# Optimization experiments

Measured on AMD Instinct MI355X. Metric: run time of the kernel, lower is better.

The kernel has to match this reference:

```python
import jax, jax.numpy as jnp
import numpy as np

B, S, E = 8, 1024, 512      # batch, seq, emb_size
L, H, K, F = 2, 4, 4, 128    # blocks, heads, conv kernel, final_size
I = 2 * E                    # inner dim (proj_factor=2)
DH = I // H                  # head dim
EPS = 1e-5


def _layernorm(x, g, b):
    mu = jnp.mean(x, axis=-1, keepdims=True)
    var = jnp.var(x, axis=-1, keepdims=True)
    return (x - mu) * jax.lax.rsqrt(var + EPS) * g + b


def _causal_conv(x, w, b):
    # x: [B,S,I], w: [K,I] depthwise, left-padded causal conv
    y = jax.lax.conv_general_dilated(
        x, w[:, None, :], window_strides=(1,), padding=[(K - 1, 0)],
        dimension_numbers=('NWC', 'WIO', 'NWC'), feature_group_count=I)
    return y + b


def _mlstm_parallel(q, k, v, ipre, fpre):
    # q,k,v: [B,H,S,DH]; ipre,fpre: [B,H,S]  (stabilized parallel mLSTM)
    lf = jax.nn.log_sigmoid(fpre)                       # [B,H,S]
    lfc = jnp.cumsum(lf, axis=-1)
    logD = lfc[..., :, None] - lfc[..., None, :] + ipre[..., None, :]  # [B,H,S,S]
    mask = jnp.tril(jnp.ones((S, S), dtype=bool))
    logD = jnp.where(mask, logD, -jnp.inf)
    m = jnp.max(logD, axis=-1, keepdims=True)           # [B,H,S,1]
    Dm = jnp.exp(logD - m)
    scores = jnp.einsum('bhtd,bhsd->bhts', q, k) * (DH ** -0.5) * Dm
    n = jnp.maximum(jnp.abs(jnp.sum(scores, axis=-1, keepdims=True)), jnp.exp(-m))
    return jnp.einsum('bhts,bhsd->bhtd', scores, v) / n


def _block(x, ln_g, ln_b, w_up, conv_w, conv_b, wq, wk, wv,
           w_i, b_i, w_f, b_f, skip, gn_g, w_down, b_down):
    res = x
    xn = _layernorm(x, ln_g, ln_b)
    up = xn @ w_up                                      # [B,S,2I]
    x_m, z = up[..., :I], up[..., I:]
    c_act = jax.nn.silu(_causal_conv(x_m, conv_w, conv_b))
    q = c_act @ wq
    k = c_act @ wk
    v = x_m @ wv
    qkv = jnp.concatenate([q, k, v], axis=-1)           # [B,S,3I]
    ipre = jnp.transpose(qkv @ w_i + b_i, (0, 2, 1))    # [B,H,S]
    fpre = jnp.transpose(qkv @ w_f + b_f, (0, 2, 1))
    to_h = lambda t: jnp.transpose(t.reshape(B, S, H, DH), (0, 2, 1, 3))
    h = _mlstm_parallel(to_h(q), to_h(k), to_h(v), ipre, fpre)  # [B,H,S,DH]
    # per-head group norm
    mu = jnp.mean(h, axis=-1, keepdims=True)
    var = jnp.var(h, axis=-1, keepdims=True)
    h = (h - mu) * jax.lax.rsqrt(var + EPS)
    h = jnp.transpose(h, (0, 2, 1, 3)).reshape(B, S, I) * gn_g
    h = h + skip * c_act
    h = h * jax.nn.silu(z)
    return res + h @ w_down + b_down


def setup_inputs() -> dict:
    key = jax.random.key(0)
    ks = jax.random.split(key, 12)
    n = lambda k, shp, s=0.02: jax.random.normal(k, shp, jnp.float32) * s
    return {
        'x': jax.random.normal(ks[0], (B, S, E), jnp.float32),
        'ln_g': jnp.ones((L, E), jnp.float32), 'ln_b': jnp.zeros((L, E), jnp.float32),
        'w_up': n(ks[1], (L, E, 2 * I)),
        'conv_w': n(ks[2], (L, K, I), 0.1), 'conv_b': jnp.zeros((L, I), jnp.float32),
        'wq': n(ks[3], (L, I, I)), 'wk': n(ks[4], (L, I, I)), 'wv': n(ks[5], (L, I, I)),
        'w_i': n(ks[6], (L, 3 * I, H)), 'b_i': jnp.zeros((L, H), jnp.float32),
        'w_f': n(ks[7], (L, 3 * I, H)), 'b_f': 3.0 * jnp.ones((L, H), jnp.float32),
        'skip': jnp.ones((L, I), jnp.float32), 'gn_g': jnp.ones((L, I), jnp.float32),
        'w_down': n(ks[8], (L, I, E)), 'b_down': jnp.zeros((L, E), jnp.float32),
        'w_fin': n(ks[9], (E, F)), 'b_fin': jnp.zeros((F,), jnp.float32),
    }


def reference(x, ln_g, ln_b, w_up, conv_w, conv_b, wq, wk, wv, w_i, b_i,
              w_f, b_f, skip, gn_g, w_down, b_down, w_fin, b_fin):
    h = x
    for l in range(L):  # 2 structurally identical mLSTM blocks
        h = _block(h, ln_g[l], ln_b[l], w_up[l], conv_w[l], conv_b[l],
                   wq[l], wk[l], wv[l], w_i[l], b_i[l], w_f[l], b_f[l],
                   skip[l], gn_g[l], w_down[l], b_down[l])
    return h @ w_fin + b_fin
```

## Files before the change

kernel.cpp:

```cpp
#include <hip/hip_runtime.h>
#include <math.h>

#define S_LEN 1024
#define I_DIM 1024
#define DH_   256
#define H_NUM 4
#define B_NUM 8
#define ROWS  (B_NUM*S_LEN)

#define GLOBAL_AS __attribute__((address_space(1)))
#define LDS_AS    __attribute__((address_space(3)))

#define VM0    asm volatile("s_waitcnt vmcnt(0)" ::: "memory")
#define LGKM0  asm volatile("s_waitcnt lgkmcnt(0)" ::: "memory")
#define BAR    __builtin_amdgcn_s_barrier()
#define SFENCE __builtin_amdgcn_sched_barrier(0)

typedef __attribute__((ext_vector_type(8))) short bf16x8;
typedef __attribute__((ext_vector_type(4))) float f32x4;
typedef unsigned short u16;

__device__ __forceinline__ u16 f2bf(float f) {
    union { float f; unsigned u; } v; v.f = f;
    unsigned r = v.u + 0x7FFF + ((v.u >> 16) & 1);
    return (u16)(r >> 16);
}
__device__ __forceinline__ float bf2f(u16 h) {
    union { unsigned u; float f; } v; v.u = ((unsigned)h) << 16;
    return v.f;
}

__global__ __launch_bounds__(64) void ln_fused_k(const float* __restrict__ x,
                                                 const float* __restrict__ g,
                                                 const float* __restrict__ b,
                                                 u16* __restrict__ out) {
    int row = blockIdx.x, lane = threadIdx.x;
    const float* xr = x + (size_t)row * 512;
    float4 a = *(const float4*)&xr[lane * 8];
    float4 c = *(const float4*)&xr[lane * 8 + 4];
    float s  = a.x + a.y + a.z + a.w + c.x + c.y + c.z + c.w;
    float s2 = a.x*a.x + a.y*a.y + a.z*a.z + a.w*a.w
             + c.x*c.x + c.y*c.y + c.z*c.z + c.w*c.w;
#pragma unroll
    for (int off = 32; off > 0; off >>= 1) {
        s  += __shfl_down(s, off);
        s2 += __shfl_down(s2, off);
    }
    s = __shfl(s, 0); s2 = __shfl(s2, 0);
    float mu = s * (1.f / 512.f);
    float rstd = rsqrtf(s2 * (1.f / 512.f) - mu * mu + 1e-5f);
    int e0 = lane * 8;
    float y[8] = {a.x,a.y,a.z,a.w,c.x,c.y,c.z,c.w};
    ushort4 o0, o1;
    o0.x = f2bf((y[0]-mu)*rstd*g[e0+0]+b[e0+0]);
    o0.y = f2bf((y[1]-mu)*rstd*g[e0+1]+b[e0+1]);
    o0.z = f2bf((y[2]-mu)*rstd*g[e0+2]+b[e0+2]);
    o0.w = f2bf((y[3]-mu)*rstd*g[e0+3]+b[e0+3]);
    o1.x = f2bf((y[4]-mu)*rstd*g[e0+4]+b[e0+4]);
    o1.y = f2bf((y[5]-mu)*rstd*g[e0+5]+b[e0+5]);
    o1.z = f2bf((y[6]-mu)*rstd*g[e0+6]+b[e0+6]);
    o1.w = f2bf((y[7]-mu)*rstd*g[e0+7]+b[e0+7]);
    *(ushort4*)&out[(size_t)row * 512 + e0]     = o0;
    *(ushort4*)&out[(size_t)row * 512 + e0 + 4] = o1;
}

__global__ __launch_bounds__(256) void cvtT_k(const float* __restrict__ W,
                                              u16* __restrict__ Wt, int K, int N) {
    __shared__ float t[32][33];
    int k0 = blockIdx.x * 32, n0 = blockIdx.y * 32;
    int c = threadIdx.x & 31, r8 = threadIdx.x >> 5;
#pragma unroll
    for (int q = 0; q < 4; q++) {
        int r = r8 * 4 + q;
        t[r][c] = W[(size_t)(k0 + r) * N + n0 + c];
    }
    __syncthreads();
#pragma unroll
    for (int q = 0; q < 4; q++) {
        int r = r8 * 4 + q;
        Wt[(size_t)(n0 + r) * K + k0 + c] = f2bf(t[c][r]);
    }
}

__global__ __launch_bounds__(256) void vt_k(const u16* __restrict__ v,
                                            u16* __restrict__ vt) {
    __shared__ u16 t[32][34];
    int s0 = blockIdx.x * 32, d0 = blockIdx.y * 32, bh = blockIdx.z;
    int b = bh >> 2, h = bh & 3;
    int c = threadIdx.x & 31, r4 = threadIdx.x >> 5;
#pragma unroll
    for (int q = 0; q < 4; q++) {
        int r = r4 * 4 + q;
        t[r][c] = v[(size_t)(b * 1024 + s0 + r) * I_DIM + h * 256 + d0 + c];
    }
    __syncthreads();
#pragma unroll
    for (int q = 0; q < 4; q++) {
        int r = r4 * 4 + q;
        vt[((size_t)bh * 256 + d0 + r) * 1024 + s0 + c] = t[c][r];
    }
}

template<int EPI>
__global__ __launch_bounds__(256) void gemm_bf16_k(
    const u16* __restrict__ A, const u16* __restrict__ Wt, int N, int K,
    float* __restrict__ Cf, u16* __restrict__ Cb,
    const float* __restrict__ bias, const float* __restrict__ res, int ldres)
{
    __shared__ __align__(16) u16 As[2][128 * 32];
    __shared__ __align__(16) u16 Bs[2][128 * 32];
    int tid = threadIdx.x;
    int lane = tid & 63;
    int wm = (tid >> 6) & 1, wn = tid >> 7;
    int gx = gridDim.x;
    int nwg = gx * gridDim.y;
    int bid = blockIdx.y * gx + blockIdx.x;
    int cpx = nwg >> 3;
    int swz = (bid & 7) * cpx + (bid >> 3);
    int r0 = (swz / gx) * 128, n0 = (swz % gx) * 128;

    int arow = tid >> 2, acol = (tid & 3) * 8;
    const u16* ap0 = A  + (size_t)(r0 + arow) * K + acol;
    const u16* ap1 = A  + (size_t)(r0 + 64 + arow) * K + acol;
    const u16* bp0 = Wt + (size_t)(n0 + arow) * K + acol;
    const u16* bp1 = Wt + (size_t)(n0 + 64 + arow) * K + acol;

    auto stage = [&](int kt, int bs) {
        int koff = kt * 32;
        __builtin_amdgcn_global_load_lds((const GLOBAL_AS unsigned int*)(ap0 + koff), (LDS_AS unsigned int*)&As[bs][tid * 8], 16, 0, 0);
        __builtin_amdgcn_global_load_lds((const GLOBAL_AS unsigned int*)(ap1 + koff), (LDS_AS unsigned int*)&As[bs][2048 + tid * 8], 16, 0, 0);
        __builtin_amdgcn_global_load_lds((const GLOBAL_AS unsigned int*)(bp0 + koff), (LDS_AS unsigned int*)&Bs[bs][tid * 8], 16, 0, 0);
        __builtin_amdgcn_global_load_lds((const GLOBAL_AS unsigned int*)(bp1 + koff), (LDS_AS unsigned int*)&Bs[bs][2048 + tid * 8], 16, 0, 0);
    };

    f32x4 acc[4][4];
#pragma unroll
    for (int i = 0; i < 4; i++)
#pragma unroll
        for (int j = 0; j < 4; j++) acc[i][j] = (f32x4){0.f, 0.f, 0.f, 0.f};

    int lm = lane & 15, lk = (lane >> 4) * 8;
    int nt = K >> 5;
    stage(0, 0);
    VM0; BAR; SFENCE;
    for (int t = 0; t < nt; ++t) {
        int cur = t & 1;
        if (t + 1 < nt) stage(t + 1, cur ^ 1);
        bf16x8 af[4], bfr[4];
#pragma unroll
        for (int f = 0; f < 4; f++) {
            af[f]  = *(const bf16x8*)&As[cur][(wm * 64 + f * 16 + lm) * 32 + lk];
            bfr[f] = *(const bf16x8*)&Bs[cur][(wn * 64 + f * 16 + lm) * 32 + lk];
        }
#pragma unroll
        for (int i = 0; i < 4; i++)
#pragma unroll
            for (int j = 0; j < 4; j++)
                acc[i][j] = __builtin_amdgcn_mfma_f32_16x16x32_bf16(af[i], bfr[j], acc[i][j], 0, 0, 0);
        VM0; BAR; SFENCE;
    }
    int lr = (lane >> 4) * 4;
#pragma unroll
    for (int i = 0; i < 4; i++) {
#pragma unroll
        for (int j = 0; j < 4; j++) {
#pragma unroll
            for (int q = 0; q < 4; q++) {
                int row = r0 + wm * 64 + i * 16 + lr + q;
                int col = n0 + wn * 64 + j * 16 + lm;
                float o = acc[i][j][q];
                if (EPI == 0) {
                    Cb[(size_t)row * N + col] = f2bf(o);
                } else if (EPI == 1) {
                    if (col < 1024) Cb[(size_t)row * 1024 + col] = f2bf(o);
                    else            Cf[(size_t)row * 1024 + (col - 1024)] = o;
                } else if (EPI == 2) {
                    o += bias[col] + res[(size_t)row * ldres + col];
                    Cf[(size_t)row * N + col] = o;
                    Cb[(size_t)row * N + col] = f2bf(o);
                } else {
                    o += bias[col];
                    Cf[(size_t)row * N + col] = o;
                }
            }
        }
    }
}

__global__ __launch_bounds__(256) void conv_k(const u16* __restrict__ xm,
                                              const float* __restrict__ w,
                                              const float* __restrict__ cb,
                                              u16* __restrict__ cact) {
    int idx = blockIdx.x * 256 + threadIdx.x;
    int r = idx >> 8;
    int c = (idx & 255) * 4;
    int t = r & 1023;
    const u16* base = xm + (size_t)(r - t) * I_DIM;
    float4 acc = *(const float4*)&cb[c];
#pragma unroll
    for (int j = 0; j < 4; j++) {
        int tt = t - 3 + j;
        if (tt >= 0) {
            short4 s = *(const short4*)&base[(size_t)tt * I_DIM + c];
            float4 wv = *(const float4*)&w[j * I_DIM + c];
            acc.x = fmaf(bf2f((u16)s.x), wv.x, acc.x);
            acc.y = fmaf(bf2f((u16)s.y), wv.y, acc.y);
            acc.z = fmaf(bf2f((u16)s.z), wv.z, acc.z);
            acc.w = fmaf(bf2f((u16)s.w), wv.w, acc.w);
        }
    }
    acc.x = acc.x / (1.f + __expf(-acc.x));
    acc.y = acc.y / (1.f + __expf(-acc.y));
    acc.z = acc.z / (1.f + __expf(-acc.z));
    acc.w = acc.w / (1.f + __expf(-acc.w));
    ushort4 o;
    o.x = f2bf(acc.x); o.y = f2bf(acc.y); o.z = f2bf(acc.z); o.w = f2bf(acc.w);
    *(ushort4*)&cact[(size_t)r * I_DIM + c] = o;
}

__global__ __launch_bounds__(256) void gates_k(const u16* __restrict__ q,
                                               const u16* __restrict__ k,
                                               const u16* __restrict__ v,
                                               const float* __restrict__ wi,
                                               const float* __restrict__ bi,
                                               const float* __restrict__ wf,
                                               const float* __restrict__ bf,
                                               float* __restrict__ ipre,
                                               float* __restrict__ fpre) {
    int r0 = blockIdx.x * 4;
    int tid = threadIdx.x;
    float ai[4][4], af4[4][4];
#pragma unroll
    for (int r = 0; r < 4; r++)
#pragma unroll
        for (int m = 0; m < 4; m++) { ai[r][m] = 0.f; af4[r][m] = 0.f; }
#pragma unroll
    for (int part = 0; part < 3; part++) {
        const u16* src = (part == 0 ? q : (part == 1 ? k : v)) + (size_t)r0 * I_DIM;
        const float* wip = wi + part * I_DIM * 4;
        const float* wfp = wf + part * I_DIM * 4;
#pragma unroll
        for (int jj = 0; jj < 4; jj++) {
            int e = tid + jj * 256;
            float4 w4  = *(const float4*)&wip[e * 4];
            float4 f4v = *(const float4*)&wfp[e * 4];
#pragma unroll
            for (int r = 0; r < 4; r++) {
                float xv = bf2f(src[(size_t)r * I_DIM + e]);
                ai[r][0] = fmaf(xv, w4.x, ai[r][0]);
                ai[r][1] = fmaf(xv, w4.y, ai[r][1]);
                ai[r][2] = fmaf(xv, w4.z, ai[r][2]);
                ai[r][3] = fmaf(xv, w4.w, ai[r][3]);
                af4[r][0] = fmaf(xv, f4v.x, af4[r][0]);
                af4[r][1] = fmaf(xv, f4v.y, af4[r][1]);
                af4[r][2] = fmaf(xv, f4v.z, af4[r][2]);
                af4[r][3] = fmaf(xv, f4v.w, af4[r][3]);
            }
        }
    }
#pragma unroll
    for (int off = 32; off > 0; off >>= 1) {
#pragma unroll
        for (int r = 0; r < 4; r++)
#pragma unroll
            for (int m = 0; m < 4; m++) {
                ai[r][m]  += __shfl_down(ai[r][m], off);
                af4[r][m] += __shfl_down(af4[r][m], off);
            }
    }
    __shared__ float red[4][32];
    int wv_ = tid >> 6, lane = tid & 63;
    if (lane == 0) {
#pragma unroll
        for (int r = 0; r < 4; r++)
#pragma unroll
            for (int m = 0; m < 4; m++) {
                red[wv_][r * 8 + m]     = ai[r][m];
                red[wv_][r * 8 + 4 + m] = af4[r][m];
            }
    }
    __syncthreads();
    if (tid < 32) {
        int r = tid >> 3, m = tid & 7;
        float s_ = red[0][tid] + red[1][tid] + red[2][tid] + red[3][tid];
        int row = r0 + r, bb = row >> 10, ss = row & 1023;
        if (m < 4) ipre[((size_t)(bb * 4 + m)) * 1024 + ss] = s_ + bi[m];
        else       fpre[((size_t)(bb * 4 + (m - 4))) * 1024 + ss] = s_ + bf[m - 4];
    }
}

__global__ __launch_bounds__(1024) void scan_k(const float* __restrict__ ipre,
                                               const float* __restrict__ fpre,
                                               float* __restrict__ cA,
                                               float* __restrict__ MA,
                                               float* __restrict__ nF) {
    __shared__ float buf[1024];
    int bh = blockIdx.x, t = threadIdx.x;
    size_t base = (size_t)bh * 1024;
    float fp = fpre[base + t];
    float lf = (fp >= 0.f) ? -log1pf(expf(-fp)) : (fp - log1pf(expf(fp)));
    buf[t] = lf; __syncthreads();
    for (int off = 1; off < 1024; off <<= 1) {
        float u = (t >= off) ? buf[t - off] : 0.f;
        __syncthreads();
        buf[t] += u;
        __syncthreads();
    }
    float lfc = buf[t];
    float c = ipre[base + t] - lfc;
    __syncthreads();
    buf[t] = c; __syncthreads();
    for (int off = 1; off < 1024; off <<= 1) {
        float u = (t >= off) ? buf[t - off] : -3.4e38f;
        __syncthreads();
        buf[t] = fmaxf(buf[t], u);
        __syncthreads();
    }
    float M = buf[t];
    cA[base + t] = c * 1.44269504f;
    MA[base + t] = M * 1.44269504f;
    nF[base + t] = expf(-(lfc + M));
}

__global__ __launch_bounds__(256) void attn_k(
    const u16* __restrict__ qg, const u16* __restrict__ kg, const u16* __restrict__ vt,
    const float* __restrict__ c2A, const float* __restrict__ M2A, const float* __restrict__ nFl,
    const u16* __restrict__ cact, const float* __restrict__ zb, u16* __restrict__ hb,
    const float* __restrict__ gng, const float* __restrict__ skip)
{
    __shared__ __align__(16) u16 Kb[2][32 * 256];
    __shared__ __align__(16) u16 Ps[64 * 40];
    __shared__ float rsI[64];
    __shared__ float gS[64 * 4];
    __shared__ float gQ[64 * 4];
    __shared__ float gmu[64], gvr[64];

    int tid = threadIdx.x;
    int w = tid >> 6, l = tid & 63;
    int lm = l & 15, lk = l >> 4;
    int b = blockIdx.z, h = blockIdx.y;
    int T0 = (15 - blockIdx.x) * 64;
    int bh32 = b * H_NUM + h;
    size_t bh = (size_t)bh32 * S_LEN;

    bf16x8 qf[8];
    {
        size_t base = ((size_t)(b * S_LEN + T0 + w * 16 + lm)) * I_DIM + h * DH_ + lk * 8;
#pragma unroll
        for (int ks = 0; ks < 8; ks++) qf[ks] = *(const bf16x8*)&qg[base + ks * 32];
    }
    f32x4 acc[4][4];
#pragma unroll
    for (int i = 0; i < 4; i++)
#pragma unroll
        for (int jd = 0; jd < 4; jd++) acc[i][jd] = (f32x4){0.f, 0.f, 0.f, 0.f};
    float rsum[2][4] = {{0,0,0,0},{0,0,0,0}};
    float m2r[4]; int tg[4];
#pragma unroll
    for (int q = 0; q < 4; q++) {
        tg[q] = T0 + w * 16 + lk * 4 + q;
        m2r[q] = M2A[bh + tg[q]];
    }

    const size_t krow0 = ((size_t)(b * S_LEN)) * I_DIM + h * DH_;
    const u16* vptr = vt + (size_t)bh32 * 256 * S_LEN + (size_t)(w * 64 + lm) * S_LEN + lk * 8;

    auto stageK = [&](int s0, int bs) {
#pragma unroll
        for (int r = 0; r < 4; r++) {
            int q = r * 256 + tid;
            int row = q >> 5, cl = q & 31;
            int cs = cl ^ (row & 7);
            const u16* src = kg + krow0 + (size_t)(s0 + row) * I_DIM + cs * 8;
            __builtin_amdgcn_global_load_lds((const GLOBAL_AS unsigned int*)src,
                                             (LDS_AS unsigned int*)&Kb[bs][q * 8], 16, 0, 0);
        }
    };

    int nst = (T0 >> 5) + 2;
    stageK(0, 0);
    bf16x8 vA[4], vB[4];
    float c2c[2], c2n[2];
#pragma unroll
    for (int jd = 0; jd < 4; jd++) vA[jd] = *(const bf16x8*)(vptr + jd * 16 * S_LEN);
    c2c[0] = c2A[bh + lm];
    c2c[1] = c2A[bh + 16 + lm];
    VM0; BAR; SFENCE;

    for (int st = 0; st < nst; st++) {
        int s0 = st * 32;
        int cur = st & 1;
        int more = (st + 1 < nst);
        if (more) {
            stageK(s0 + 32, cur ^ 1);
#pragma unroll
            for (int jd = 0; jd < 4; jd++) vB[jd] = *(const bf16x8*)(vptr + jd * 16 * S_LEN + s0 + 32);
            c2n[0] = c2A[bh + s0 + 32 + lm];
            c2n[1] = c2A[bh + s0 + 48 + lm];
        }
        f32x4 sacc[2];
        sacc[0] = (f32x4){0.f,0.f,0.f,0.f};
        sacc[1] = (f32x4){0.f,0.f,0.f,0.f};
        __builtin_amdgcn_s_setprio(1);
#pragma unroll
        for (int ks = 0; ks < 8; ks++) {
#pragma unroll
            for (int js = 0; js < 2; js++) {
                int row = js * 16 + lm;
                int ch = (ks * 4 + lk) ^ (row & 7);
                bf16x8 kf = *(const bf16x8*)&Kb[cur][row * 256 + ch * 8];
                sacc[js] = __builtin_amdgcn_mfma_f32_16x16x32_bf16(qf[ks], kf, sacc[js], 0, 0, 0);
            }
        }
        __builtin_amdgcn_s_setprio(0);
#pragma unroll
        for (int js = 0; js < 2; js++) {
            int sg = s0 + js * 16 + lm;
#pragma unroll
            for (int q = 0; q < 4; q++) {
                float v = sacc[js][q] * 0.0625f * __builtin_amdgcn_exp2f(c2c[js] - m2r[q]);
                v = (sg <= tg[q]) ? v : 0.f;
                u16 pb = f2bf(v);
                rsum[js][q] += bf2f(pb);
                Ps[(w * 16 + lk * 4 + q) * 40 + js * 16 + lm] = pb;
            }
        }
        LGKM0; BAR; SFENCE;
        __builtin_amdgcn_s_setprio(1);
#pragma unroll
        for (int i = 0; i < 4; i++) {
            bf16x8 pa = *(const bf16x8*)&Ps[(i * 16 + lm) * 40 + lk * 8];
#pragma unroll
            for (int jd = 0; jd < 4; jd++)
                acc[i][jd] = __builtin_amdgcn_mfma_f32_16x16x32_bf16(pa, vA[jd], acc[i][jd], 0, 0, 0);
        }
        __builtin_amdgcn_s_setprio(0);
        VM0; BAR; SFENCE;
        if (more) {
#pragma unroll
            for (int jd = 0; jd < 4; jd++) vA[jd] = vB[jd];
            c2c[0] = c2n[0]; c2c[1] = c2n[1];
        }
    }
    {
        float rq[4];
#pragma unroll
        for (int q = 0; q < 4; q++) rq[q] = rsum[0][q] + rsum[1][q];
#pragma unroll
        for (int m = 1; m < 16; m <<= 1) {
#pragma unroll
            for (int q = 0; q < 4; q++) rq[q] += __shfl_xor(rq[q], m);
        }
        if (lm == 0) {
#pragma unroll
            for (int q = 0; q < 4; q++) rsI[w * 16 + lk * 4 + q] = rq[q];
        }
    }
    __syncthreads();
    if (tid < 64) {
        float n = fmaxf(fabsf(rsI[tid]), nFl[bh + T0 + tid]);
        rsI[tid] = 1.f / n;
    }
    __syncthreads();
#pragma unroll
    for (int i = 0; i < 4; i++) {
#pragma unroll
        for (int q = 0; q < 4; q++) {
            int rl = i * 16 + lk * 4 + q;
            float inv = rsI[rl];
            float ps = 0.f, pq = 0.f;
#pragma unroll
            for (int jd = 0; jd < 4; jd++) {
                float v = acc[i][jd][q] * inv;
                acc[i][jd][q] = v;
                ps += v; pq += v * v;
            }
#pragma unroll
            for (int m = 1; m < 16; m <<= 1) {
                ps += __shfl_xor(ps, m);
                pq += __shfl_xor(pq, m);
            }
            if (lm == 0) { gS[rl * 4 + w] = ps; gQ[rl * 4 + w] = pq; }
        }
    }
    __syncthreads();
    if (tid < 64) {
        float s1 = gS[tid*4] + gS[tid*4+1] + gS[tid*4+2] + gS[tid*4+3];
        float s2 = gQ[tid*4] + gQ[tid*4+1] + gQ[tid*4+2] + gQ[tid*4+3];
        float mu = s1 * (1.f / 256.f);
        float var = s2 * (1.f / 256.f) - mu * mu;
        gmu[tid] = mu;
        gvr[tid] = rsqrtf(var + 1e-5f);
    }
    __syncthreads();
#pragma unroll
    for (int i = 0; i < 4; i++) {
#pragma unroll
        for (int q = 0; q < 4; q++) {
            int rl = i * 16 + lk * 4 + q;
            size_t r = (size_t)b * S_LEN + T0 + rl;
            float mu = gmu[rl], rv = gvr[rl];
#pragma unroll
            for (int jd = 0; jd < 4; jd++) {
                int cix = h * DH_ + w * 64 + jd * 16 + lm;
                float val = (acc[i][jd][q] - mu) * rv * gng[cix];
                float ca = bf2f(cact[r * I_DIM + cix]);
                float z = zb[r * I_DIM + cix];
                float hm = (val + skip[cix] * ca) * (z / (1.f + __expf(-z)));
                hb[r * I_DIM + cix] = f2bf(hm);
            }
        }
    }
}

extern "C" void kernel_launch(void* const* d_in, const int* in_sizes, int n_in,
                              void* d_out, int out_size, void* d_ws, size_t ws_size,
                              hipStream_t stream) {
    const float* x      = (const float*)d_in[0];
    const float* ln_g   = (const float*)d_in[1];
    const float* ln_b   = (const float*)d_in[2];
    const float* w_up   = (const float*)d_in[3];
    const float* conv_w = (const float*)d_in[4];
    const float* conv_b = (const float*)d_in[5];
    const float* wq     = (const float*)d_in[6];
    const float* wk     = (const float*)d_in[7];
    const float* wv     = (const float*)d_in[8];
    const float* w_i    = (const float*)d_in[9];
    const float* b_i    = (const float*)d_in[10];
    const float* w_f    = (const float*)d_in[11];
    const float* b_f    = (const float*)d_in[12];
    const float* skip   = (const float*)d_in[13];
    const float* gn_g   = (const float*)d_in[14];
    const float* w_down = (const float*)d_in[15];
    const float* b_down = (const float*)d_in[16];
    const float* w_fin  = (const float*)d_in[17];
    const float* b_fin  = (const float*)d_in[18];

    char* p = (char*)d_ws;
    auto alloc = [&](size_t bytes) { void* r = p; p += (bytes + 255) & ~(size_t)255; return r; };
    float* zbuf  = (float*)alloc((size_t)ROWS * 1024 * 4);
    float* xa    = (float*)alloc((size_t)ROWS * 512 * 4);
    float* xb2   = (float*)alloc((size_t)ROWS * 512 * 4);
    u16*  xln    = (u16*)alloc((size_t)ROWS * 512 * 2);
    u16*  xm     = (u16*)alloc((size_t)ROWS * 1024 * 2);
    u16*  cactb  = (u16*)alloc((size_t)ROWS * 1024 * 2);
    u16*  qbf    = (u16*)alloc((size_t)ROWS * 1024 * 2);
    u16*  kbf    = (u16*)alloc((size_t)ROWS * 1024 * 2);
    u16*  vbf    = (u16*)alloc((size_t)ROWS * 1024 * 2);
    u16*  vtg    = (u16*)alloc((size_t)32 * 256 * 1024 * 2);
    u16*  hbf    = (u16*)alloc((size_t)ROWS * 1024 * 2);
    u16*  xoutb  = (u16*)alloc((size_t)ROWS * 512 * 2);
    u16*  wupT   = (u16*)alloc((size_t)2 * 2048 * 512 * 2);
    u16*  wqT    = (u16*)alloc((size_t)2 * 1024 * 1024 * 2);
    u16*  wkT    = (u16*)alloc((size_t)2 * 1024 * 1024 * 2);
    u16*  wvT    = (u16*)alloc((size_t)2 * 1024 * 1024 * 2);
    u16*  wdT    = (u16*)alloc((size_t)2 * 512 * 1024 * 2);
    u16*  wfT    = (u16*)alloc((size_t)128 * 512 * 2);
    float* ipre  = (float*)alloc(32768 * 4);
    float* fpre  = (float*)alloc(32768 * 4);
    float* cA    = (float*)alloc(32768 * 4);
    float* MA    = (float*)alloc(32768 * 4);
    float* nF    = (float*)alloc(32768 * 4);

    for (int l = 0; l < 2; l++) {
        cvtT_k<<<dim3(16, 64), 256, 0, stream>>>(w_up + (size_t)l * 512 * 2048, wupT + (size_t)l * 2048 * 512, 512, 2048);
        cvtT_k<<<dim3(32, 32), 256, 0, stream>>>(wq + (size_t)l * 1024 * 1024, wqT + (size_t)l * 1024 * 1024, 1024, 1024);
        cvtT_k<<<dim3(32, 32), 256, 0, stream>>>(wk + (size_t)l * 1024 * 1024, wkT + (size_t)l * 1024 * 1024, 1024, 1024);
        cvtT_k<<<dim3(32, 32), 256, 0, stream>>>(wv + (size_t)l * 1024 * 1024, wvT + (size_t)l * 1024 * 1024, 1024, 1024);
        cvtT_k<<<dim3(32, 16), 256, 0, stream>>>(w_down + (size_t)l * 1024 * 512, wdT + (size_t)l * 512 * 1024, 1024, 512);
    }
    cvtT_k<<<dim3(16, 4), 256, 0, stream>>>(w_fin, wfT, 512, 128);

    const float* xin = x;
    for (int l = 0; l < 2; l++) {
        float* xout = (l == 0) ? xa : xb2;
        ln_fused_k<<<ROWS, 64, 0, stream>>>(xin, ln_g + l * 512, ln_b + l * 512, xln);
        gemm_bf16_k<1><<<dim3(16, 64), 256, 0, stream>>>(
            xln, wupT + (size_t)l * 2048 * 512, 2048, 512, zbuf, xm, nullptr, nullptr, 0);
        conv_k<<<ROWS, 256, 0, stream>>>(xm, conv_w + l * 4 * I_DIM, conv_b + l * I_DIM, cactb);
        gemm_bf16_k<0><<<dim3(8, 64), 256, 0, stream>>>(
            xm, wvT + (size_t)l * 1024 * 1024, 1024, 1024, nullptr, vbf, nullptr, nullptr, 0);
        gemm_bf16_k<0><<<dim3(8, 64), 256, 0, stream>>>(
            cactb, wqT + (size_t)l * 1024 * 1024, 1024, 1024, nullptr, qbf, nullptr, nullptr, 0);
        gemm_bf16_k<0><<<dim3(8, 64), 256, 0, stream>>>(
            cactb, wkT + (size_t)l * 1024 * 1024, 1024, 1024, nullptr, kbf, nullptr, nullptr, 0);
        vt_k<<<dim3(32, 8, 32), 256, 0, stream>>>(vbf, vtg);
        gates_k<<<ROWS / 4, 256, 0, stream>>>(qbf, kbf, vbf,
            w_i + l * 3072 * 4, b_i + l * 4, w_f + l * 3072 * 4, b_f + l * 4, ipre, fpre);
        scan_k<<<32, 1024, 0, stream>>>(ipre, fpre, cA, MA, nF);
        attn_k<<<dim3(16, 4, 8), 256, 0, stream>>>(qbf, kbf, vtg, cA, MA, nF, cactb, zbuf, hbf,
            gn_g + l * I_DIM, skip + l * I_DIM);
        gemm_bf16_k<2><<<dim3(4, 64), 256, 0, stream>>>(
            hbf, wdT + (size_t)l * 512 * 1024, 512, 1024, xout, xoutb,
            b_down + l * 512, xin, 512);
        xin = xout;
    }
    gemm_bf16_k<3><<<dim3(1, 64), 256, 0, stream>>>(
        xoutb, wfT, 128, 512, (float*)d_out, nullptr, b_fin, nullptr, 0);
}
```

Before: 693.9 us.

## Fuse Q/K projections into one GEMM and halve attention query tile

```diff
diff --git a/kernel.cpp b/kernel.cpp
--- a/kernel.cpp
+++ b/kernel.cpp
@@ -218,8 +218,7 @@
     *(ushort4*)&cact[(size_t)r * I_DIM + c] = o;
 }
 
-__global__ __launch_bounds__(256) void gates_k(const u16* __restrict__ q,
-                                               const u16* __restrict__ k,
+__global__ __launch_bounds__(256) void gates_k(const u16* __restrict__ qk,
                                                const u16* __restrict__ v,
                                                const float* __restrict__ wi,
                                                const float* __restrict__ bi,
@@ -236,7 +235,10 @@
         for (int m = 0; m < 4; m++) { ai[r][m] = 0.f; af4[r][m] = 0.f; }
 #pragma unroll
     for (int part = 0; part < 3; part++) {
-        const u16* src = (part == 0 ? q : (part == 1 ? k : v)) + (size_t)r0 * I_DIM;
+        const u16* src; size_t st;
+        if (part == 0)      { src = qk + (size_t)r0 * 2048;        st = 2048; }
+        else if (part == 1) { src = qk + (size_t)r0 * 2048 + 1024; st = 2048; }
+        else                { src = v  + (size_t)r0 * 1024;        st = 1024; }
         const float* wip = wi + part * I_DIM * 4;
         const float* wfp = wf + part * I_DIM * 4;
 #pragma unroll
@@ -246,7 +248,7 @@
             float4 f4v = *(const float4*)&wfp[e * 4];
 #pragma unroll
             for (int r = 0; r < 4; r++) {
-                float xv = bf2f(src[(size_t)r * I_DIM + e]);
+                float xv = bf2f(src[(size_t)r * st + e]);
                 ai[r][0] = fmaf(xv, w4.x, ai[r][0]);
                 ai[r][1] = fmaf(xv, w4.y, ai[r][1]);
                 ai[r][2] = fmaf(xv, w4.z, ai[r][2]);
@@ -329,40 +331,44 @@
     const float* __restrict__ gng, const float* __restrict__ skip)
 {
     __shared__ __align__(16) u16 Kb[2][32 * 256];
-    __shared__ __align__(16) u16 Ps[64 * 40];
-    __shared__ float rsI[64];
-    __shared__ float gS[64 * 4];
-    __shared__ float gQ[64 * 4];
-    __shared__ float gmu[64], gvr[64];
+    __shared__ __align__(16) u16 Ps[32 * 40];
+    __shared__ float rs2[4][16];
+    __shared__ float rsI[32];
+    __shared__ float gS[32 * 4];
+    __shared__ float gQ[32 * 4];
+    __shared__ float gmu[32], gvr[32];
 
     int tid = threadIdx.x;
     int w = tid >> 6, l = tid & 63;
     int lm = l & 15, lk = l >> 4;
-    int b = blockIdx.z, h = blockIdx.y;
-    int T0 = (15 - blockIdx.x) * 64;
+    int i0 = blockIdx.x;
+    int g = (i0 & 7) * 128 + (i0 >> 3);
+    int b = g >> 7, h = (g >> 5) & 3, bx = g & 31;
+    int T0 = (31 - bx) * 32;
+    int tf = w & 1, sf = w >> 1;
     int bh32 = b * H_NUM + h;
     size_t bh = (size_t)bh32 * S_LEN;
 
     bf16x8 qf[8];
     {
-        size_t base = ((size_t)(b * S_LEN + T0 + w * 16 + lm)) * I_DIM + h * DH_ + lk * 8;
+        size_t base = ((size_t)(b * S_LEN + T0 + tf * 16 + lm)) * 2048 + h * DH_ + lk * 8;
 #pragma unroll
         for (int ks = 0; ks < 8; ks++) qf[ks] = *(const bf16x8*)&qg[base + ks * 32];
     }
-    f32x4 acc[4][4];
-#pragma unroll
-    for (int i = 0; i < 4; i++)
+    f32x4 acc[2][4];
+#pragma unroll
+    for (int i = 0; i < 2; i++)
 #pragma unroll
         for (int jd = 0; jd < 4; jd++) acc[i][jd] = (f32x4){0.f, 0.f, 0.f, 0.f};
-    float rsum[2][4] = {{0,0,0,0},{0,0,0,0}};
+    float rsum[4] = {0, 0, 0, 0};
     float m2r[4]; int tg[4];
 #pragma unroll
     for (int q = 0; q < 4; q++) {
-        tg[q] = T0 + w * 16 + lk * 4 + q;
+        tg[q] = T0 + tf * 16 + lk * 4 + q;
         m2r[q] = M2A[bh + tg[q]];
     }
 
-    const size_t krow0 = ((size_t)(b * S_LEN)) * I_DIM + h * DH_;
+    const size_t krow0 = (size_t)(b * S_LEN) * 2048 + h * DH_;
     const u16* vptr = vt + (size_t)bh32 * 256 * S_LEN + (size_t)(w * 64 + lm) * S_LEN + lk * 8;
 
     auto stageK = [&](int s0, int bs) {
@@ -371,20 +377,19 @@
             int q = r * 256 + tid;
             int row = q >> 5, cl = q & 31;
             int cs = cl ^ (row & 7);
-            const u16* src = kg + krow0 + (size_t)(s0 + row) * I_DIM + cs * 8;
+            const u16* src = kg + krow0 + (size_t)(s0 + row) * 2048 + cs * 8;
             __builtin_amdgcn_global_load_lds((const GLOBAL_AS unsigned int*)src,
                                              (LDS_AS unsigned int*)&Kb[bs][q * 8], 16, 0, 0);
         }
     };
 
-    int nst = (T0 >> 5) + 2;
+    int nst = (T0 >> 5) + 1;
     stageK(0, 0);
     bf16x8 vA[4], vB[4];
-    float c2c[2], c2n[2];
+    float c2c, c2n;
 #pragma unroll
     for (int jd = 0; jd < 4; jd++) vA[jd] = *(const bf16x8*)(vptr + jd * 16 * S_LEN);
-    c2c[0] = c2A[bh + lm];
-    c2c[1] = c2A[bh + 16 + lm];
+    c2c = c2A[bh + sf * 16 + lm];
     VM0; BAR; SFENCE;
 
     for (int st = 0; st < nst; st++) {
@@ -395,40 +400,33 @@
             stageK(s0 + 32, cur ^ 1);
 #pragma unroll
             for (int jd = 0; jd < 4; jd++) vB[jd] = *(const bf16x8*)(vptr + jd * 16 * S_LEN + s0 + 32);
-            c2n[0] = c2A[bh + s0 + 32 + lm];
-            c2n[1] = c2A[bh + s0 + 48 + lm];
-        }
-        f32x4 sacc[2];
-        sacc[0] = (f32x4){0.f,0.f,0.f,0.f};
-        sacc[1] = (f32x4){0.f,0.f,0.f,0.f};
+            c2n = c2A[bh + s0 + 32 + sf * 16 + lm];
+        }
+        f32x4 sacc = (f32x4){0.f, 0.f, 0.f, 0.f};
         __builtin_amdgcn_s_setprio(1);
 #pragma unroll
         for (int ks = 0; ks < 8; ks++) {
-#pragma unroll
-            for (int js = 0; js < 2; js++) {
-                int row = js * 16 + lm;
-                int ch = (ks * 4 + lk) ^ (row & 7);
-                bf16x8 kf = *(const bf16x8*)&Kb[cur][row * 256 + ch * 8];
-                sacc[js] = __builtin_amdgcn_mfma_f32_16x16x32_bf16(qf[ks], kf, sacc[js], 0, 0, 0);
-            }
+            int row = sf * 16 + lm;
+            int ch = (ks * 4 + lk) ^ (row & 7);
+            bf16x8 kf = *(const bf16x8*)&Kb[cur][row * 256 + ch * 8];
+            sacc = __builtin_amdgcn_mfma_f32_16x16x32_bf16(qf[ks], kf, sacc, 0, 0, 0);
         }
         __builtin_amdgcn_s_setprio(0);
-#pragma unroll
-        for (int js = 0; js < 2; js++) {
-            int sg = s0 + js * 16 + lm;
+        {
+            int sg = s0 + sf * 16 + lm;
 #pragma unroll
             for (int q = 0; q < 4; q++) {
-                float v = sacc[js][q] * 0.0625f * __builtin_amdgcn_exp2f(c2c[js] - m2r[q]);
+                float v = sacc[q] * 0.0625f * __builtin_amdgcn_exp2f(c2c - m2r[q]);
                 v = (sg <= tg[q]) ? v : 0.f;
                 u16 pb = f2bf(v);
-                rsum[js][q] += bf2f(pb);
-                Ps[(w * 16 + lk * 4 + q) * 40 + js * 16 + lm] = pb;
+                rsum[q] += bf2f(pb);
+                Ps[(tf * 16 + lk * 4 + q) * 40 + sf * 16 + lm] = pb;
             }
         }
         LGKM0; BAR; SFENCE;
         __builtin_amdgcn_s_setprio(1);
 #pragma unroll
-        for (int i = 0; i < 4; i++) {
+        for (int i = 0; i < 2; i++) {
             bf16x8 pa = *(const bf16x8*)&Ps[(i * 16 + lm) * 40 + lk * 8];
 #pragma unroll
             for (int jd = 0; jd < 4; jd++)
@@ -439,31 +437,30 @@
         if (more) {
 #pragma unroll
             for (int jd = 0; jd < 4; jd++) vA[jd] = vB[jd];
-            c2c[0] = c2n[0]; c2c[1] = c2n[1];
+            c2c = c2n;
         }
     }
     {
-        float rq[4];
-#pragma unroll
-        for (int q = 0; q < 4; q++) rq[q] = rsum[0][q] + rsum[1][q];
 #pragma unroll
         for (int m = 1; m < 16; m <<= 1) {
 #pragma unroll
-            for (int q = 0; q < 4; q++) rq[q] += __shfl_xor(rq[q], m);
+            for (int q = 0; q < 4; q++) rsum[q] += __shfl_xor(rsum[q], m);
         }
         if (lm == 0) {
 #pragma unroll
-            for (int q = 0; q < 4; q++) rsI[w * 16 + lk * 4 + q] = rq[q];
-        }
-    }
-    __syncthreads();
-    if (tid < 64) {
-        float n = fmaxf(fabsf(rsI[tid]), nFl[bh + T0 + tid]);
+            for (int q = 0; q < 4; q++) rs2[w][lk * 4 + q] = rsum[q];
+        }
+    }
+    __syncthreads();
+    if (tid < 32) {
+        int tfi = tid >> 4, idx = tid & 15;
+        float s = rs2[tfi][idx] + rs2[tfi + 2][idx];
+        float n = fmaxf(fabsf(s), nFl[bh + T0 + tid]);
         rsI[tid] = 1.f / n;
     }
     __syncthreads();
 #pragma unroll
-    for (int i = 0; i < 4; i++) {
+    for (int i = 0; i < 2; i++) {
 #pragma unroll
         for (int q = 0; q < 4; q++) {
             int rl = i * 16 + lk * 4 + q;
@@ -484,7 +481,7 @@
         }
     }
     __syncthreads();
-    if (tid < 64) {
+    if (tid < 32) {
         float s1 = gS[tid*4] + gS[tid*4+1] + gS[tid*4+2] + gS[tid*4+3];
         float s2 = gQ[tid*4] + gQ[tid*4+1] + gQ[tid*4+2] + gQ[tid*4+3];
         float mu = s1 * (1.f / 256.f);
@@ -494,7 +491,7 @@
     }
     __syncthreads();
 #pragma unroll
-    for (int i = 0; i < 4; i++) {
+    for (int i = 0; i < 2; i++) {
 #pragma unroll
         for (int q = 0; q < 4; q++) {
             int rl = i * 16 + lk * 4 + q;
@@ -544,15 +541,13 @@
     u16*  xln    = (u16*)alloc((size_t)ROWS * 512 * 2);
     u16*  xm     = (u16*)alloc((size_t)ROWS * 1024 * 2);
     u16*  cactb  = (u16*)alloc((size_t)ROWS * 1024 * 2);
-    u16*  qbf    = (u16*)alloc((size_t)ROWS * 1024 * 2);
-    u16*  kbf    = (u16*)alloc((size_t)ROWS * 1024 * 2);
+    u16*  qkbf   = (u16*)alloc((size_t)ROWS * 2048 * 2);
     u16*  vbf    = (u16*)alloc((size_t)ROWS * 1024 * 2);
     u16*  vtg    = (u16*)alloc((size_t)32 * 256 * 1024 * 2);
     u16*  hbf    = (u16*)alloc((size_t)ROWS * 1024 * 2);
     u16*  xoutb  = (u16*)alloc((size_t)ROWS * 512 * 2);
     u16*  wupT   = (u16*)alloc((size_t)2 * 2048 * 512 * 2);
-    u16*  wqT    = (u16*)alloc((size_t)2 * 1024 * 1024 * 2);
-    u16*  wkT    = (u16*)alloc((size_t)2 * 1024 * 1024 * 2);
+    u16*  wqkT   = (u16*)alloc((size_t)2 * 2048 * 1024 * 2);
     u16*  wvT    = (u16*)alloc((size_t)2 * 1024 * 1024 * 2);
     u16*  wdT    = (u16*)alloc((size_t)2 * 512 * 1024 * 2);
     u16*  wfT    = (u16*)alloc((size_t)128 * 512 * 2);
@@ -564,8 +559,8 @@
 
     for (int l = 0; l < 2; l++) {
         cvtT_k<<<dim3(16, 64), 256, 0, stream>>>(w_up + (size_t)l * 512 * 2048, wupT + (size_t)l * 2048 * 512, 512, 2048);
-        cvtT_k<<<dim3(32, 32), 256, 0, stream>>>(wq + (size_t)l * 1024 * 1024, wqT + (size_t)l * 1024 * 1024, 1024, 1024);
-        cvtT_k<<<dim3(32, 32), 256, 0, stream>>>(wk + (size_t)l * 1024 * 1024, wkT + (size_t)l * 1024 * 1024, 1024, 1024);
+        cvtT_k<<<dim3(32, 32), 256, 0, stream>>>(wq + (size_t)l * 1024 * 1024, wqkT + (size_t)l * 2048 * 1024, 1024, 1024);
+        cvtT_k<<<dim3(32, 32), 256, 0, stream>>>(wk + (size_t)l * 1024 * 1024, wqkT + (size_t)l * 2048 * 1024 + 1024 * 1024, 1024, 1024);
         cvtT_k<<<dim3(32, 32), 256, 0, stream>>>(wv + (size_t)l * 1024 * 1024, wvT + (size_t)l * 1024 * 1024, 1024, 1024);
         cvtT_k<<<dim3(32, 16), 256, 0, stream>>>(w_down + (size_t)l * 1024 * 512, wdT + (size_t)l * 512 * 1024, 1024, 512);
     }
@@ -580,15 +575,13 @@
         conv_k<<<ROWS, 256, 0, stream>>>(xm, conv_w + l * 4 * I_DIM, conv_b + l * I_DIM, cactb);
         gemm_bf16_k<0><<<dim3(8, 64), 256, 0, stream>>>(
             xm, wvT + (size_t)l * 1024 * 1024, 1024, 1024, nullptr, vbf, nullptr, nullptr, 0);
-        gemm_bf16_k<0><<<dim3(8, 64), 256, 0, stream>>>(
-            cactb, wqT + (size_t)l * 1024 * 1024, 1024, 1024, nullptr, qbf, nullptr, nullptr, 0);
-        gemm_bf16_k<0><<<dim3(8, 64), 256, 0, stream>>>(
-            cactb, wkT + (size_t)l * 1024 * 1024, 1024, 1024, nullptr, kbf, nullptr, nullptr, 0);
+        gemm_bf16_k<0><<<dim3(16, 64), 256, 0, stream>>>(
+            cactb, wqkT + (size_t)l * 2048 * 1024, 2048, 1024, nullptr, qkbf, nullptr, nullptr, 0);
         vt_k<<<dim3(32, 8, 32), 256, 0, stream>>>(vbf, vtg);
-        gates_k<<<ROWS / 4, 256, 0, stream>>>(qbf, kbf, vbf,
+        gates_k<<<ROWS / 4, 256, 0, stream>>>(qkbf, vbf,
             w_i + l * 3072 * 4, b_i + l * 4, w_f + l * 3072 * 4, b_f + l * 4, ipre, fpre);
         scan_k<<<32, 1024, 0, stream>>>(ipre, fpre, cA, MA, nF);
-        attn_k<<<dim3(16, 4, 8), 256, 0, stream>>>(qbf, kbf, vtg, cA, MA, nF, cactb, zbuf, hbf,
+        attn_k<<<dim3(1024), 256, 0, stream>>>(qkbf, qkbf + 1024, vtg, cA, MA, nF, cactb, zbuf, hbf,
             gn_g + l * I_DIM, skip + l * I_DIM);
         gemm_bf16_k<2><<<dim3(4, 64), 256, 0, stream>>>(
             hbf, wdT + (size_t)l * 512 * 1024, 512, 1024, xout, xoutb,
```

Result: slower. 714.9 us (+3.0%).
